# Kernel optimization log

Hardware: AMD Instinct MI355X
Metric: run time of the kernel (lower is better)

## Reference

```python
import jax, jax.numpy as jnp
import numpy as np

D_MODEL = 1024
N_HEAD = 16
SEQ = 4096
BATCH = 1


def setup_inputs() -> dict:
    key = jax.random.key(0)
    k1, k2, k3 = jax.random.split(key, 3)
    scale_in = 1.0 / np.sqrt(D_MODEL)
    x = jax.random.normal(k1, (BATCH, SEQ, D_MODEL), dtype=jnp.float32)
    # torch nn.Linear(d, 3d, bias=False): y = x @ W.T with W [3d, d].
    # We store the transposed matrix [d, 3d] so y = x @ w_qkv (same math).
    w_qkv = jax.random.normal(k2, (D_MODEL, 3 * D_MODEL), dtype=jnp.float32) * scale_in
    w_proj = jax.random.normal(k3, (D_MODEL, D_MODEL), dtype=jnp.float32) * scale_in
    return {"x": x, "w_qkv": w_qkv, "w_proj": w_proj}


def _attention(x, w_qkv, w_proj):
    bsz, t, c = x.shape
    d_head = c // N_HEAD
    qkv = x @ w_qkv                              # [b, t, 3c]
    q, k, v = jnp.split(qkv, 3, axis=-1)

    def reshape(tensor):
        # [b, t, c] -> [b, h, t, d]
        return tensor.reshape(bsz, t, N_HEAD, d_head).transpose(0, 2, 1, 3)

    q, k, v = reshape(q), reshape(k), reshape(v)
    scale = 1.0 / jnp.sqrt(jnp.asarray(d_head, dtype=q.dtype))
    scores = jnp.einsum("bhqd,bhkd->bhqk", q, k) * scale  # [b, h, t, t]
    causal = jnp.tril(jnp.ones((t, t), dtype=bool))
    scores = jnp.where(causal, scores, jnp.asarray(-jnp.inf, dtype=scores.dtype))
    attn = jax.nn.softmax(scores, axis=-1)
    y = jnp.einsum("bhqk,bhkd->bhqd", attn, v)            # [b, h, t, d]
    y = y.transpose(0, 2, 1, 3).reshape(bsz, t, c)        # [b, t, c]
    return y @ w_proj


def reference(x, w_qkv, w_proj):
    return _attention(x, w_qkv, w_proj)
```

## Files before the change

### kernel.cpp

```cpp
#include <hip/hip_runtime.h>
#include <hip/hip_bf16.h>


typedef unsigned short ushort_t;
typedef __attribute__((ext_vector_type(8))) __bf16 bf16x8;
typedef __attribute__((ext_vector_type(8))) unsigned short ushort8;
typedef __attribute__((ext_vector_type(4))) unsigned short ushort4v;
typedef __attribute__((ext_vector_type(2))) unsigned short ushort2v;
typedef __attribute__((ext_vector_type(4))) float f32x4;

#define SWZ(row, e) (((row) << 6) + ((e) ^ (((row) & 7) << 3)))

__device__ inline unsigned short f2bf(float f) {
  union { float f; unsigned int u; } v;
  v.f = f;
  unsigned int r = v.u + 0x7fffu + ((v.u >> 16) & 1u);
  return (unsigned short)(r >> 16);
}

__device__ __forceinline__ float fast_exp2(float x) {
  float r;
  asm("v_exp_f32 %0, %1" : "=v"(r) : "v"(x));
  return r;
}

__device__ __forceinline__ void gl_lds16(const void* g, void* l) {
  __builtin_amdgcn_global_load_lds((const __attribute__((address_space(1))) void*)g,
                                   (__attribute__((address_space(3))) void*)l, 16, 0, 0);
}

__global__ __launch_bounds__(256) void prep(const float* __restrict__ x,
                                            ushort_t* __restrict__ xb,
                                            const float* __restrict__ w_qkv,
                                            ushort_t* __restrict__ wqkvT,
                                            const float* __restrict__ w_proj,
                                            ushort_t* __restrict__ wprojT) {
  const int b = blockIdx.x;
  const int tid = threadIdx.x;
  if (b < 4096) {
    const size_t i = ((size_t)b * 256 + tid) * 4;
    const float4 v = *(const float4*)(x + i);
    ushort4v o;
    o.x = f2bf(v.x); o.y = f2bf(v.y); o.z = f2bf(v.z); o.w = f2bf(v.w);
    *(ushort4v*)(xb + i) = o;
  } else {
    __shared__ ushort_t tile[32][33];
    const float* in;
    ushort_t* out;
    int R, C, bx, by;
    if (b < 7168) {
      const int bb = b - 4096;
      bx = bb % 96; by = bb / 96; in = w_qkv; out = wqkvT; R = 1024; C = 3072;
    } else {
      const int bb = b - 7168;
      bx = bb % 32; by = bb / 32; in = w_proj; out = wprojT; R = 1024; C = 1024;
    }
    const int r0 = by * 32, c0 = bx * 32;
    const int tx = tid & 31, ty = tid >> 5;
    #pragma unroll
    for (int j = 0; j < 32; j += 8)
      tile[ty + j][tx] = f2bf(in[(size_t)(r0 + ty + j) * C + c0 + tx]);
    __syncthreads();
    #pragma unroll
    for (int j = 0; j < 32; j += 8)
      out[(size_t)(c0 + ty + j) * R + r0 + tx] = tile[tx][ty + j];
  }
}

__global__ __launch_bounds__(256, 3) void gemm_bt_bf16out(const ushort_t* __restrict__ A,
                                                          const ushort_t* __restrict__ Bt,
                                                          ushort_t* __restrict__ C,
                                                          ushort_t* __restrict__ vT,
                                                          int M, int N, int K) {
  __shared__ __attribute__((aligned(16))) ushort_t smem[128 * 64 * 2];
  ushort_t* As = smem;
  ushort_t* Bs = smem + 128 * 64;
  const int tid = threadIdx.x;
  const int lane = tid & 63;
  const int wave = tid >> 6;
  const int wy = wave >> 1, wx = wave & 1;
  const int quad = lane >> 4, l16 = lane & 15;
  const int bid = blockIdx.y * 24 + blockIdx.x;
  const int xcd = bid & 7, j = bid >> 3;
  const int bxp = (xcd & 1) * 12 + (j >> 3);
  const int byp = (xcd >> 1) * 8 + (j & 7);
  const size_t bm = (size_t)byp * 128;
  const size_t bn = (size_t)bxp * 128;

  const f32x4 fzero = {0.f, 0.f, 0.f, 0.f};
  f32x4 acc[4][4];
  #pragma unroll
  for (int i = 0; i < 4; ++i)
    #pragma unroll
    for (int jj = 0; jj < 4; ++jj) acc[i][jj] = fzero;

  for (int k0 = 0; k0 < K; k0 += 64) {
    #pragma unroll
    for (int i = 0; i < 4; ++i) {
      int c = (wave * 4 + i) * 64 + lane;
      int row = c >> 3, col = (c & 7) * 8;
      gl_lds16(A + (bm + row) * K + k0 + col, As + c * 8);
      gl_lds16(Bt + (bn + row) * K + k0 + col, Bs + c * 8);
    }
    __syncthreads();
    #pragma unroll
    for (int ks = 0; ks < 2; ++ks) {
      bf16x8 af[4], bb[4];
      #pragma unroll
      for (int mt = 0; mt < 4; ++mt)
        af[mt] = *(const bf16x8*)(As + (wy * 64 + mt * 16 + l16) * 64 + ks * 32 + quad * 8);
      #pragma unroll
      for (int nt = 0; nt < 4; ++nt)
        bb[nt] = *(const bf16x8*)(Bs + (wx * 64 + nt * 16 + l16) * 64 + ks * 32 + quad * 8);
      #pragma unroll
      for (int mt = 0; mt < 4; ++mt)
        #pragma unroll
        for (int nt = 0; nt < 4; ++nt)
          acc[mt][nt] = __builtin_amdgcn_mfma_f32_16x16x32_bf16(af[mt], bb[nt], acc[mt][nt], 0, 0, 0);
    }
    __syncthreads();
  }

  if (bxp < 16) {
    const float sc = (bxp < 8) ? 0.18033688f : 1.0f;
    #pragma unroll
    for (int mt = 0; mt < 4; ++mt)
      #pragma unroll
      for (int nt = 0; nt < 4; ++nt)
        #pragma unroll
        for (int r = 0; r < 4; ++r)
          C[(bm + wy * 64 + mt * 16 + quad * 4 + r) * N + bn + wx * 64 + nt * 16 + l16] =
              f2bf(acc[mt][nt][r] * sc);
  } else {
    const int vbase = (int)bn - 2048;
    #pragma unroll
    for (int p = 0; p < 2; ++p) {
      if (wx == p) {
        #pragma unroll
        for (int nt = 0; nt < 4; ++nt)
          #pragma unroll
          for (int mt = 0; mt < 4; ++mt)
            #pragma unroll
            for (int i = 0; i < 2; ++i) {
              ushort2v pr;
              pr.x = f2bf(acc[mt][nt][2 * i]);
              pr.y = f2bf(acc[mt][nt][2 * i + 1]);
              *(ushort2v*)(smem + (nt * 16 + l16) * 136 + wy * 64 + mt * 16 + quad * 4 +
                           2 * i) = pr;
            }
      }
      __syncthreads();
      #pragma unroll
      for (int jj = 0; jj < 4; ++jj) {
        int v = (tid >> 4) + jj * 16;
        int row0 = (tid & 15) * 8;
        ushort8 val = *(const ushort8*)(smem + v * 136 + row0);
        *(ushort8*)(vT + (size_t)(vbase + p * 64 + v) * 4096 + bm + row0) = val;
      }
      __syncthreads();
    }
  }
}

__global__ __launch_bounds__(256, 2) void gemm_bt_f32out(const ushort_t* __restrict__ A,
                                                         const ushort_t* __restrict__ Bt,
                                                         float* __restrict__ C,
                                                         int M, int N, int K, int lda) {
  __shared__ __attribute__((aligned(16))) ushort_t As[128 * 64];
  __shared__ __attribute__((aligned(16))) ushort_t Bs[64 * 64];
  const int tid = threadIdx.x;
  const int lane = tid & 63;
  const int wave = tid >> 6;
  const int wy = wave >> 1, wx = wave & 1;
  const int quad = lane >> 4, l16 = lane & 15;
  const int bid = blockIdx.y * 16 + blockIdx.x;
  const int xcd = bid & 7, j = bid >> 3;
  const int bxp = (xcd & 1) * 8 + (j >> 3);
  const int byp = (xcd >> 1) * 8 + (j & 7);
  const size_t bm = (size_t)byp * 128;
  const size_t bn = (size_t)bxp * 64;

  const f32x4 fzero = {0.f, 0.f, 0.f, 0.f};
  f32x4 acc[4][2];
  #pragma unroll
  for (int i = 0; i < 4; ++i)
    #pragma unroll
    for (int jj = 0; jj < 2; ++jj) acc[i][jj] = fzero;

  for (int k0 = 0; k0 < K; k0 += 64) {
    #pragma unroll
    for (int i = 0; i < 4; ++i) {
      int c = (wave * 4 + i) * 64 + lane;
      int row = c >> 3, col = (c & 7) * 8;
      gl_lds16(A + (bm + row) * lda + k0 + col, As + c * 8);
    }
    #pragma unroll
    for (int i = 0; i < 2; ++i) {
      int c = (wave * 2 + i) * 64 + lane;
      int row = c >> 3, col = (c & 7) * 8;
      gl_lds16(Bt + (bn + row) * K + k0 + col, Bs + c * 8);
    }
    __syncthreads();
    #pragma unroll
    for (int ks = 0; ks < 2; ++ks) {
      bf16x8 af[4], bb[2];
      #pragma unroll
      for (int mt = 0; mt < 4; ++mt)
        af[mt] = *(const bf16x8*)(As + (wy * 64 + mt * 16 + l16) * 64 + ks * 32 + quad * 8);
      #pragma unroll
      for (int nt = 0; nt < 2; ++nt)
        bb[nt] = *(const bf16x8*)(Bs + (wx * 32 + nt * 16 + l16) * 64 + ks * 32 + quad * 8);
      #pragma unroll
      for (int mt = 0; mt < 4; ++mt)
        #pragma unroll
        for (int nt = 0; nt < 2; ++nt)
          acc[mt][nt] = __builtin_amdgcn_mfma_f32_16x16x32_bf16(af[mt], bb[nt], acc[mt][nt], 0, 0, 0);
    }
    __syncthreads();
  }
  #pragma unroll
  for (int mt = 0; mt < 4; ++mt)
    #pragma unroll
    for (int nt = 0; nt < 2; ++nt)
      #pragma unroll
      for (int r = 0; r < 4; ++r)
        C[(bm + wy * 64 + mt * 16 + quad * 4 + r) * N + bn + wx * 32 + nt * 16 + l16] =
            acc[mt][nt][r];
}

__global__ __launch_bounds__(256, 4) void attn_fwd(const ushort_t* __restrict__ qkv,
                                                   const ushort_t* __restrict__ vT,
                                                   ushort_t* __restrict__ y) {
  __shared__ __attribute__((aligned(16))) ushort_t Ks[2][64 * 64];
  __shared__ __attribute__((aligned(16))) ushort_t Vt[2][64 * 64];
  __shared__ __attribute__((aligned(16))) ushort_t Ps[64 * 64];
  const int head = blockIdx.x;
  const int by = blockIdx.y;
  const int g = by >> 4, r4 = by & 15;
  const int qt = (g == 0) ? r4 : (g == 1) ? (63 - r4) : (g == 2) ? (16 + r4) : (47 - r4);
  const int qb = qt * 64;
  const int ntiles = qt + 1;
  const int tid = threadIdx.x;
  const int lane = tid & 63, wave = tid >> 6;
  const int quad = lane >> 4, l16 = lane & 15;
  const int hoff = head * 64;
  const int wrow = wave * 16;
  const int srow = tid >> 2, scol = (tid & 3) * 16;

  bf16x8 bq[4][2];
  #pragma unroll
  for (int q2 = 0; q2 < 4; ++q2)
    #pragma unroll
    for (int ks = 0; ks < 2; ++ks)
      bq[q2][ks] = *(const bf16x8*)(qkv + (size_t)(qb + q2 * 16 + l16) * 3072 + hoff +
                                    ks * 32 + quad * 8);

  bf16x8 ones;
  #pragma unroll
  for (int i = 0; i < 8; ++i) ones[i] = (__bf16)1.0f;

  ushort8 kreg[2], vreg[2];
  #pragma unroll
  for (int i = 0; i < 2; ++i) {
    kreg[i] = *(const ushort8*)(qkv + (size_t)srow * 3072 + 1024 + hoff + scol + i * 8);
    vreg[i] = *(const ushort8*)(vT + (size_t)(hoff + srow) * 4096 + scol + i * 8);
  }
  #pragma unroll
  for (int i = 0; i < 2; ++i) {
    *(ushort8*)(Ks[0] + SWZ(srow, scol + i * 8)) = kreg[i];
    *(ushort8*)(Vt[0] + SWZ(srow, scol + i * 8)) = vreg[i];
  }
  #pragma unroll
  for (int i = 0; i < 2; ++i) {
    kreg[i] = *(const ushort8*)(qkv + (size_t)(64 + srow) * 3072 + 1024 + hoff + scol + i * 8);
    vreg[i] = *(const ushort8*)(vT + (size_t)(hoff + srow) * 4096 + 64 + scol + i * 8);
  }

  const f32x4 fzero = {0.f, 0.f, 0.f, 0.f};
  f32x4 o0[4], ol0 = fzero;
  #pragma unroll
  for (int nt = 0; nt < 4; ++nt) o0[nt] = fzero;

  for (int t = 0; t < ntiles; ++t) {
    const int cur = t & 1;
    __syncthreads();

    f32x4 s[4];
    #pragma unroll
    for (int q2 = 0; q2 < 4; ++q2) s[q2] = fzero;
    bf16x8 ak[2];
    #pragma unroll
    for (int ks = 0; ks < 2; ++ks)
      ak[ks] = *(const bf16x8*)(Ks[cur] + SWZ(wrow + l16, ks * 32 + quad * 8));
    __builtin_amdgcn_s_setprio(1);
    #pragma unroll
    for (int ks = 0; ks < 2; ++ks)
      #pragma unroll
      for (int q2 = 0; q2 < 4; ++q2)
        s[q2] = __builtin_amdgcn_mfma_f32_16x16x32_bf16(ak[ks], bq[q2][ks], s[q2], 0, 0, 0);
    __builtin_amdgcn_s_setprio(0);

    if (t + 1 < ntiles) {
      #pragma unroll
      for (int i = 0; i < 2; ++i) {
        *(ushort8*)(Ks[1 - cur] + SWZ(srow, scol + i * 8)) = kreg[i];
        *(ushort8*)(Vt[1 - cur] + SWZ(srow, scol + i * 8)) = vreg[i];
      }
      if (t + 2 < ntiles) {
        const int kb2 = (t + 2) * 64;
        #pragma unroll
        for (int i = 0; i < 2; ++i) {
          kreg[i] = *(const ushort8*)(qkv + (size_t)(kb2 + srow) * 3072 + 1024 + hoff +
                                      scol + i * 8);
          vreg[i] = *(const ushort8*)(vT + (size_t)(hoff + srow) * 4096 + kb2 + scol + i * 8);
        }
      }
    }

    const int kb = t * 64;
    const bool masked = (kb + 63 > qb);
    #pragma unroll
    for (int q2 = 0; q2 < 4; ++q2) {
      float p[4];
      #pragma unroll
      for (int r = 0; r < 4; ++r) {
        float xv = s[q2][r];
        if (masked) {
          int kkg = kb + wrow + quad * 4 + r;
          xv = (kkg <= qb + q2 * 16 + l16) ? xv : -30000.f;
        }
        p[r] = fast_exp2(xv);
      }
      unsigned int u01, u23;
      asm("v_cvt_pk_bf16_f32 %0, %1, %2" : "=v"(u01) : "v"(p[0]), "v"(p[1]));
      asm("v_cvt_pk_bf16_f32 %0, %1, %2" : "=v"(u23) : "v"(p[2]), "v"(p[3]));
      uint2 pu; pu.x = u01; pu.y = u23;
      *(uint2*)(Ps + SWZ(q2 * 16 + l16, wrow + quad * 4)) = pu;
    }

    __syncthreads();

    __builtin_amdgcn_s_setprio(1);
    #pragma unroll
    for (int ks = 0; ks < 2; ++ks) {
      bf16x8 bp0 = *(const bf16x8*)(Ps + SWZ(wrow + l16, ks * 32 + quad * 8));
      #pragma unroll
      for (int nt = 0; nt < 4; ++nt) {
        bf16x8 av = *(const bf16x8*)(Vt[cur] + SWZ(nt * 16 + l16, ks * 32 + quad * 8));
        o0[nt] = __builtin_amdgcn_mfma_f32_16x16x32_bf16(av, bp0, o0[nt], 0, 0, 0);
      }
      ol0 = __builtin_amdgcn_mfma_f32_16x16x32_bf16(ones, bp0, ol0, 0, 0, 0);
    }
    __builtin_amdgcn_s_setprio(0);
  }

  const float inv0 = 1.0f / ol0[0];
  #pragma unroll
  for (int nt = 0; nt < 4; ++nt) {
    ushort4v ov0;
    #pragma unroll
    for (int r = 0; r < 4; ++r) ov0[r] = f2bf(o0[nt][r] * inv0);
    *(ushort4v*)(y + (size_t)(qb + wrow + l16) * 3072 + hoff + nt * 16 + quad * 4) = ov0;
  }
}

extern "C" void kernel_launch(void* const* d_in, const int* in_sizes, int n_in,
                              void* d_out, int out_size, void* d_ws, size_t ws_size,
                              hipStream_t stream) {
  const float* x = (const float*)d_in[0];
  const float* w_qkv = (const float*)d_in[1];
  const float* w_proj = (const float*)d_in[2];
  float* out = (float*)d_out;

  ushort_t* ws = (ushort_t*)d_ws;
  ushort_t* qkv = ws;
  ushort_t* wqkvT = ws + (size_t)4096 * 3072;
  ushort_t* wprojT = wqkvT + (size_t)3072 * 1024;
  ushort_t* yb = qkv + 2048;
  ushort_t* xb = (ushort_t*)d_out;
  ushort_t* vT = (ushort_t*)d_out + (size_t)4096 * 1024;

  prep<<<8192, 256, 0, stream>>>(x, xb, w_qkv, wqkvT, w_proj, wprojT);
  gemm_bt_bf16out<<<dim3(24, 32), 256, 0, stream>>>(xb, wqkvT, qkv, vT, 4096, 3072, 1024);
  attn_fwd<<<dim3(16, 64), 256, 0, stream>>>(qkv, vT, yb);
  gemm_bt_f32out<<<dim3(16, 32), 256, 0, stream>>>(yb, wprojT, out, 4096, 1024, 1024, 3072);
}
```

Baseline: 195.6 us.

## Double-buffer LDS in both GEMMs and vectorize weight transpose stores

Both GEMM kernels now stage tiles into two LDS buffers, so the global-to-LDS load for the next K step is issued while MFMAs run on the current buffer. This removes one barrier per iteration and hides load latency. MFMA blocks are wrapped in s_setprio, and the launch-bounds occupancy hints are adjusted to fit the doubled LDS. The weight-transpose kernel now writes two bf16 values per store instead of one. The trade-off is doubled LDS per block, which may lower occupancy.

```diff
diff --git a/kernel.cpp b/kernel.cpp
--- a/kernel.cpp
+++ b/kernel.cpp
@@ -61,20 +61,25 @@
     for (int j = 0; j < 32; j += 8)
       tile[ty + j][tx] = f2bf(in[(size_t)(r0 + ty + j) * C + c0 + tx]);
     __syncthreads();
-    #pragma unroll
-    for (int j = 0; j < 32; j += 8)
-      out[(size_t)(c0 + ty + j) * R + r0 + tx] = tile[tx][ty + j];
-  }
-}
-
-__global__ __launch_bounds__(256, 3) void gemm_bt_bf16out(const ushort_t* __restrict__ A,
+    const int txh = tid & 15, tyw = tid >> 4;
+    #pragma unroll
+    for (int j = 0; j < 32; j += 16) {
+      const int c = tyw + j;
+      ushort2v o;
+      o.x = tile[2 * txh][c];
+      o.y = tile[2 * txh + 1][c];
+      *(ushort2v*)(out + (size_t)(c0 + c) * R + r0 + 2 * txh) = o;
+    }
+  }
+}
+
+__global__ __launch_bounds__(256, 2) void gemm_bt_bf16out(const ushort_t* __restrict__ A,
                                                           const ushort_t* __restrict__ Bt,
                                                           ushort_t* __restrict__ C,
                                                           ushort_t* __restrict__ vT,
                                                           int M, int N, int K) {
-  __shared__ __attribute__((aligned(16))) ushort_t smem[128 * 64 * 2];
-  ushort_t* As = smem;
-  ushort_t* Bs = smem + 128 * 64;
+  __shared__ __attribute__((aligned(16))) ushort_t As[2][128 * 64];
+  __shared__ __attribute__((aligned(16))) ushort_t Bs[2][128 * 64];
   const int tid = threadIdx.x;
   const int lane = tid & 63;
   const int wave = tid >> 6;
@@ -87,38 +92,50 @@
   const size_t bm = (size_t)byp * 128;
   const size_t bn = (size_t)bxp * 128;
 
-  const f32x4 fzero = {0.f, 0.f, 0.f, 0.f};
-  f32x4 acc[4][4];
-  #pragma unroll
-  for (int i = 0; i < 4; ++i)
-    #pragma unroll
-    for (int jj = 0; jj < 4; ++jj) acc[i][jj] = fzero;
-
-  for (int k0 = 0; k0 < K; k0 += 64) {
+  auto stage = [&](int buf, int k0) {
     #pragma unroll
     for (int i = 0; i < 4; ++i) {
       int c = (wave * 4 + i) * 64 + lane;
       int row = c >> 3, col = (c & 7) * 8;
-      gl_lds16(A + (bm + row) * K + k0 + col, As + c * 8);
-      gl_lds16(Bt + (bn + row) * K + k0 + col, Bs + c * 8);
-    }
-    __syncthreads();
+      gl_lds16(A + (bm + row) * K + k0 + col, &As[buf][c * 8]);
+      gl_lds16(Bt + (bn + row) * K + k0 + col, &Bs[buf][c * 8]);
+    }
+  };
+
+  const f32x4 fzero = {0.f, 0.f, 0.f, 0.f};
+  f32x4 acc[4][4];
+  #pragma unroll
+  for (int i = 0; i < 4; ++i)
+    #pragma unroll
+    for (int jj = 0; jj < 4; ++jj) acc[i][jj] = fzero;
+
+  stage(0, 0);
+  asm volatile("s_waitcnt vmcnt(0)" ::: "memory");
+  __syncthreads();
+
+  int cur = 0;
+  for (int k0 = 0; k0 < K; k0 += 64) {
+    if (k0 + 64 < K) stage(cur ^ 1, k0 + 64);
     #pragma unroll
     for (int ks = 0; ks < 2; ++ks) {
       bf16x8 af[4], bb[4];
       #pragma unroll
       for (int mt = 0; mt < 4; ++mt)
-        af[mt] = *(const bf16x8*)(As + (wy * 64 + mt * 16 + l16) * 64 + ks * 32 + quad * 8);
+        af[mt] = *(const bf16x8*)(&As[cur][(wy * 64 + mt * 16 + l16) * 64 + ks * 32 + quad * 8]);
       #pragma unroll
       for (int nt = 0; nt < 4; ++nt)
-        bb[nt] = *(const bf16x8*)(Bs + (wx * 64 + nt * 16 + l16) * 64 + ks * 32 + quad * 8);
+        bb[nt] = *(const bf16x8*)(&Bs[cur][(wx * 64 + nt * 16 + l16) * 64 + ks * 32 + quad * 8]);
+      __builtin_amdgcn_s_setprio(1);
       #pragma unroll
       for (int mt = 0; mt < 4; ++mt)
         #pragma unroll
         for (int nt = 0; nt < 4; ++nt)
           acc[mt][nt] = __builtin_amdgcn_mfma_f32_16x16x32_bf16(af[mt], bb[nt], acc[mt][nt], 0, 0, 0);
-    }
+      __builtin_amdgcn_s_setprio(0);
+    }
+    asm volatile("s_waitcnt vmcnt(0)" ::: "memory");
     __syncthreads();
+    cur ^= 1;
   }
 
   if (bxp < 16) {
@@ -132,6 +149,7 @@
           C[(bm + wy * 64 + mt * 16 + quad * 4 + r) * N + bn + wx * 64 + nt * 16 + l16] =
               f2bf(acc[mt][nt][r] * sc);
   } else {
+    ushort_t* smem = &As[0][0];
     const int vbase = (int)bn - 2048;
     #pragma unroll
     for (int p = 0; p < 2; ++p) {
@@ -162,12 +180,12 @@
   }
 }
 
-__global__ __launch_bounds__(256, 2) void gemm_bt_f32out(const ushort_t* __restrict__ A,
+__global__ __launch_bounds__(256, 3) void gemm_bt_f32out(const ushort_t* __restrict__ A,
                                                          const ushort_t* __restrict__ Bt,
                                                          float* __restrict__ C,
                                                          int M, int N, int K, int lda) {
-  __shared__ __attribute__((aligned(16))) ushort_t As[128 * 64];
-  __shared__ __attribute__((aligned(16))) ushort_t Bs[64 * 64];
+  __shared__ __attribute__((aligned(16))) ushort_t As[2][128 * 64];
+  __shared__ __attribute__((aligned(16))) ushort_t Bs[2][64 * 64];
   const int tid = threadIdx.x;
   const int lane = tid & 63;
   const int wave = tid >> 6;
@@ -180,43 +198,55 @@
   const size_t bm = (size_t)byp * 128;
   const size_t bn = (size_t)bxp * 64;
 
-  const f32x4 fzero = {0.f, 0.f, 0.f, 0.f};
-  f32x4 acc[4][2];
-  #pragma unroll
-  for (int i = 0; i < 4; ++i)
-    #pragma unroll
-    for (int jj = 0; jj < 2; ++jj) acc[i][jj] = fzero;
-
-  for (int k0 = 0; k0 < K; k0 += 64) {
+  auto stage = [&](int buf, int k0) {
     #pragma unroll
     for (int i = 0; i < 4; ++i) {
       int c = (wave * 4 + i) * 64 + lane;
       int row = c >> 3, col = (c & 7) * 8;
-      gl_lds16(A + (bm + row) * lda + k0 + col, As + c * 8);
+      gl_lds16(A + (bm + row) * lda + k0 + col, &As[buf][c * 8]);
     }
     #pragma unroll
     for (int i = 0; i < 2; ++i) {
       int c = (wave * 2 + i) * 64 + lane;
       int row = c >> 3, col = (c & 7) * 8;
-      gl_lds16(Bt + (bn + row) * K + k0 + col, Bs + c * 8);
-    }
-    __syncthreads();
+      gl_lds16(Bt + (bn + row) * K + k0 + col, &Bs[buf][c * 8]);
+    }
+  };
+
+  const f32x4 fzero = {0.f, 0.f, 0.f, 0.f};
+  f32x4 acc[4][2];
+  #pragma unroll
+  for (int i = 0; i < 4; ++i)
+    #pragma unroll
+    for (int jj = 0; jj < 2; ++jj) acc[i][jj] = fzero;
+
+  stage(0, 0);
+  asm volatile("s_waitcnt vmcnt(0)" ::: "memory");
+  __syncthreads();
+
+  int cur = 0;
+  for (int k0 = 0; k0 < K; k0 += 64) {
+    if (k0 + 64 < K) stage(cur ^ 1, k0 + 64);
     #pragma unroll
     for (int ks = 0; ks < 2; ++ks) {
       bf16x8 af[4], bb[2];
       #pragma unroll
       for (int mt = 0; mt < 4; ++mt)
-        af[mt] = *(const bf16x8*)(As + (wy * 64 + mt * 16 + l16) * 64 + ks * 32 + quad * 8);
+        af[mt] = *(const bf16x8*)(&As[cur][(wy * 64 + mt * 16 + l16) * 64 + ks * 32 + quad * 8]);
       #pragma unroll
       for (int nt = 0; nt < 2; ++nt)
-        bb[nt] = *(const bf16x8*)(Bs + (wx * 32 + nt * 16 + l16) * 64 + ks * 32 + quad * 8);
+        bb[nt] = *(const bf16x8*)(&Bs[cur][(wx * 32 + nt * 16 + l16) * 64 + ks * 32 + quad * 8]);
+      __builtin_amdgcn_s_setprio(1);
       #pragma unroll
       for (int mt = 0; mt < 4; ++mt)
         #pragma unroll
         for (int nt = 0; nt < 2; ++nt)
           acc[mt][nt] = __builtin_amdgcn_mfma_f32_16x16x32_bf16(af[mt], bb[nt], acc[mt][nt], 0, 0, 0);
-    }
+      __builtin_amdgcn_s_setprio(0);
+    }
+    asm volatile("s_waitcnt vmcnt(0)" ::: "memory");
     __syncthreads();
+    cur ^= 1;
   }
   #pragma unroll
   for (int mt = 0; mt < 4; ++mt)
```

New measurement: 211.9 us. 1.08x slower.
